# Kernel tuning notes

Measured on AMD Instinct MI355X. Metric: run time of the kernel, lower is better.

Reference implementation:

```python
import jax, jax.numpy as jnp
import numpy as np

N = 50000      # num nodes
EG = 1600000   # num edges (avg degree 32)
IN = 64        # in_dim
OUT = 64       # out_dim
H = 4          # num_heads
D = OUT // H   # per-head dim


def setup_inputs() -> dict:
    key = jax.random.key(0)
    ks = jax.random.split(key, 12)
    s = 1.0 / np.sqrt(IN)
    return {
        "x": jax.random.normal(ks[0], (N, IN), jnp.float32),
        "edge_attr": jax.random.normal(ks[1], (EG, IN), jnp.float32),
        "edge_index": jax.random.randint(ks[2], (2, EG), 0, N, jnp.int32),
        "Wq": jax.random.uniform(ks[3], (OUT, IN), jnp.float32, -s, s),
        "bq": jax.random.uniform(ks[4], (OUT,), jnp.float32, -s, s),
        "Wk": jax.random.uniform(ks[5], (OUT, IN), jnp.float32, -s, s),
        "bk": jax.random.uniform(ks[6], (OUT,), jnp.float32, -s, s),
        "We": jax.random.uniform(ks[7], (OUT, IN), jnp.float32, -s, s),
        "be": jax.random.uniform(ks[8], (OUT,), jnp.float32, -s, s),
        "Wv": jax.random.uniform(ks[9], (OUT, IN), jnp.float32, -s, s),
        "bv": jax.random.uniform(ks[10], (OUT,), jnp.float32, -s, s),
    }


def reference(x, edge_attr, edge_index, Wq, bq, Wk, bk, We, be, Wv, bv):
    n = x.shape[0]
    # linear projections, reshaped to [*, H, D]
    Qh = (x @ Wq.T + bq).reshape(n, H, D)
    Kh = (x @ Wk.T + bk).reshape(n, H, D)
    Vh = (x @ Wv.T + bv).reshape(n, H, D)
    Ee = (edge_attr @ We.T + be).reshape(-1, H, D)
    src = edge_index[0]
    dst = edge_index[1]
    # per-edge score: sum_d K[src] * Q[dst] / sqrt(D) * E  -> [E, H]
    score = ((Kh[src] * Qh[dst]) * (1.0 / np.sqrt(D)) * Ee).sum(-1)
    score = jnp.exp(jnp.clip(score, -5.0, 5.0))            # [E, H]
    msg = Vh[src] * score[..., None]                        # [E, H, D]
    wV = jax.ops.segment_sum(msg, dst, num_segments=n)      # [N, H, D]
    # note: original forward returns wV without dividing by Z
    return wV.reshape(n, H * D)
```

## Files before the change

### kernel.cpp

```cpp
#include <hip/hip_runtime.h>


typedef __attribute__((ext_vector_type(8))) short bf16x8;
typedef __attribute__((ext_vector_type(4))) float f32x4;
union frag_u { uint32_t u[4]; uint4 u4; bf16x8 v; };

__device__ __forceinline__ uint32_t pack2(float a, float b) {
    return (__float_as_uint(a) >> 16) | (__float_as_uint(b) & 0xffff0000u);
}
__device__ __forceinline__ void cvt4(float4 v, uint32_t& h0, uint32_t& h1,
                                     uint32_t& l0, uint32_t& l1) {
    float hx = __uint_as_float(__float_as_uint(v.x) & 0xffff0000u);
    float hy = __uint_as_float(__float_as_uint(v.y) & 0xffff0000u);
    float hz = __uint_as_float(__float_as_uint(v.z) & 0xffff0000u);
    float hw = __uint_as_float(__float_as_uint(v.w) & 0xffff0000u);
    h0 = pack2(v.x, v.y);
    h1 = pack2(v.z, v.w);
    l0 = pack2(v.x - hx, v.y - hy);
    l1 = pack2(v.z - hz, v.w - hw);
}

__global__ __launch_bounds__(256) void proj_kernel(
    const float* __restrict__ x,
    const float* __restrict__ Wq, const float* __restrict__ bq,
    const float* __restrict__ Wk, const float* __restrict__ bk,
    const float* __restrict__ Wv, const float* __restrict__ bv,
    const int* __restrict__ ei, int* __restrict__ cnt,
    float* __restrict__ Qb, float* __restrict__ KV,
    int n, int EG)
{
    __shared__ float WqT[64 * 65];
    __shared__ float WkT[64 * 65];
    __shared__ float WvT[64 * 65];
    __shared__ float xs[4][4][64];

    const int tid  = threadIdx.x;
    const int wave = tid >> 6;
    const int lane = tid & 63;

    #pragma unroll
    for (int k = 0; k < 16; ++k) {
        int idx = tid + k * 256;
        int j = idx >> 6, i = idx & 63;
        WqT[i * 65 + j] = Wq[idx];
        WkT[i * 65 + j] = Wk[idx];
        WvT[i * 65 + j] = Wv[idx];
    }
    const float bqv = bq[lane];
    const float bkv = bk[lane];
    const float bvv = bv[lane];
    __syncthreads();

    for (int blockbase = blockIdx.x * 16; blockbase < n;
         blockbase += gridDim.x * 16) {
        int base = blockbase + wave * 4;
        #pragma unroll
        for (int j = 0; j < 4; ++j) {
            int node = base + j;
            xs[wave][j][lane] = (node < n) ? x[node * 64 + lane] : 0.f;
        }
        __syncthreads();

        float accq[4], acck[4], accv[4];
        #pragma unroll
        for (int j = 0; j < 4; ++j) { accq[j] = bqv; acck[j] = bkv; accv[j] = bvv; }

        #pragma unroll
        for (int f = 0; f < 16; ++f) {
            float wq[4], wk[4], wv[4];
            #pragma unroll
            for (int u = 0; u < 4; ++u) {
                int i = 4 * f + u;
                wq[u] = WqT[i * 65 + lane];
                wk[u] = WkT[i * 65 + lane];
                wv[u] = WvT[i * 65 + lane];
            }
            #pragma unroll
            for (int j = 0; j < 4; ++j) {
                float4 xv = *reinterpret_cast<const float4*>(&xs[wave][j][4 * f]);
                accq[j] = fmaf(xv.x, wq[0], accq[j]);
                accq[j] = fmaf(xv.y, wq[1], accq[j]);
                accq[j] = fmaf(xv.z, wq[2], accq[j]);
                accq[j] = fmaf(xv.w, wq[3], accq[j]);
                acck[j] = fmaf(xv.x, wk[0], acck[j]);
                acck[j] = fmaf(xv.y, wk[1], acck[j]);
                acck[j] = fmaf(xv.z, wk[2], acck[j]);
                acck[j] = fmaf(xv.w, wk[3], acck[j]);
                accv[j] = fmaf(xv.x, wv[0], accv[j]);
                accv[j] = fmaf(xv.y, wv[1], accv[j]);
                accv[j] = fmaf(xv.z, wv[2], accv[j]);
                accv[j] = fmaf(xv.w, wv[3], accv[j]);
            }
        }

        #pragma unroll
        for (int j = 0; j < 4; ++j) {
            int node = base + j;
            if (node < n) {
                Qb[(size_t)node * 64 + lane]       = accq[j];
                KV[(size_t)node * 128 + lane]      = acck[j];
                KV[(size_t)node * 128 + 64 + lane] = accv[j];
            }
        }
        __syncthreads();
    }

    {
        const int nt4 = EG >> 2;
        int i  = blockIdx.x * blockDim.x + threadIdx.x;
        int st = gridDim.x * blockDim.x;
        const int4* d4 = reinterpret_cast<const int4*>(ei + EG);
        for (int e = i; e < nt4; e += st) {
            int4 d = d4[e];
            atomicAdd(&cnt[d.x], 1);
            atomicAdd(&cnt[d.y], 1);
            atomicAdd(&cnt[d.z], 1);
            atomicAdd(&cnt[d.w], 1);
        }
    }
}

__global__ __launch_bounds__(256) void scanA_kernel(
    const int* __restrict__ cnt, int* __restrict__ off,
    int* __restrict__ bsum, int n)
{
    __shared__ int s[256];
    const int t = threadIdx.x;
    const int i = blockIdx.x * 256 + t;
    const int v = (i < n) ? cnt[i] : 0;
    s[t] = v;
    __syncthreads();
    for (int d = 1; d < 256; d <<= 1) {
        int u = (t >= d) ? s[t - d] : 0;
        __syncthreads();
        s[t] += u;
        __syncthreads();
    }
    if (i < n) off[i] = s[t] - v;
    if (t == 255) bsum[blockIdx.x] = s[255];
}

__global__ __launch_bounds__(256) void scanB_kernel(int* __restrict__ bsum, int nb)
{
    __shared__ int s[256];
    const int t = threadIdx.x;
    const int v = (t < nb) ? bsum[t] : 0;
    s[t] = v;
    __syncthreads();
    for (int d = 1; d < 256; d <<= 1) {
        int u = (t >= d) ? s[t - d] : 0;
        __syncthreads();
        s[t] += u;
        __syncthreads();
    }
    if (t < nb) bsum[t] = s[t] - v;
}

__global__ __launch_bounds__(256) void scanC_kernel(
    int* __restrict__ off, const int* __restrict__ bsum,
    int* __restrict__ cursor, int n, int EG)
{
    const int i = blockIdx.x * 256 + threadIdx.x;
    if (i < n) {
        int v = off[i] + bsum[blockIdx.x];
        off[i] = v;
        cursor[i] = v;
    }
    if (i == 0) off[n] = EG;
}

__global__ __launch_bounds__(256) void scatter_kernel(
    const int* __restrict__ ei, int* __restrict__ cursor,
    int* __restrict__ perm, int EG)
{
    int i  = blockIdx.x * blockDim.x + threadIdx.x;
    int st = gridDim.x * blockDim.x;
    for (int e = i; e < EG; e += st) {
        int d = ei[EG + e];
        int p = atomicAdd(&cursor[d], 1);
        perm[p] = e;
    }
}

__global__ __launch_bounds__(256) void agg_kernel(
    const float* __restrict__ ea, const int* __restrict__ ei,
    const int* __restrict__ off, const int* __restrict__ perm,
    const float* __restrict__ Qb, const float* __restrict__ KV,
    const float* __restrict__ We, const float* __restrict__ be,
    float* __restrict__ out, int n, int EG)
{
    __shared__ uint4 bfragLDS[16][64];
    __shared__ int sidt[4][16];
    __shared__ int eidt[4][16];

    const int tid  = threadIdx.x;
    const int wave = __builtin_amdgcn_readfirstlane(tid >> 6);
    const int lane = tid & 63;
    const int g    = lane >> 4;
    const int q    = lane & 15;

    {
        const int nt = wave;
        #pragma unroll
        for (int ks = 0; ks < 2; ++ks) {
            frag_u fh, fl;
            #pragma unroll
            for (int b = 0; b < 2; ++b) {
                float4 w4 = *reinterpret_cast<const float4*>(
                    &We[(size_t)(16 * nt + q) * 64 + 32 * ks + 16 * b + 4 * g]);
                cvt4(w4, fh.u[2 * b + 0], fh.u[2 * b + 1],
                         fl.u[2 * b + 0], fl.u[2 * b + 1]);
            }
            bfragLDS[nt * 4 + ks * 2 + 0][lane] = fh.u4;
            bfragLDS[nt * 4 + ks * 2 + 1][lane] = fl.u4;
        }
    }
    float bias4[4];
    #pragma unroll
    for (int nt = 0; nt < 4; ++nt) bias4[nt] = be[16 * nt + q];
    __syncthreads();

    const int nw  = gridDim.x * 4;
    const int nd4 = n >> 2;

    for (int wid = blockIdx.x * 4 + wave; wid < nd4; wid += nw) {
        const int dbase = wid << 2;
        const int mydst = dbase + g;
        const int j0  = off[mydst];
        const int j1  = off[mydst + 1];
        const int deg = j1 - j0;

        float qreg[4];
        #pragma unroll
        for (int nt = 0; nt < 4; ++nt)
            qreg[nt] = Qb[(size_t)mydst * 64 + 16 * nt + q];

        const int grp  = (lane & 15) >> 2;
        const int slot = lane & 3;
        const int j0p  = __shfl(j0, grp << 4);
        const int j1p  = __shfl(j1, grp << 4);

        int dm = max(deg, __shfl_xor(deg, 16));
        dm = max(dm, __shfl_xor(dm, 32));
        const int iters = __builtin_amdgcn_readfirstlane((dm + 3) >> 2);

        float macc[4] = {0.f, 0.f, 0.f, 0.f};

        for (int c = 0; c < iters; ++c) {
            if (lane < 16) {
                const int  p     = j0p + 4 * c + slot;
                const bool valid = p < j1p;
                const int  eid   = valid ? perm[p] : 0;
                const int  src   = valid ? ei[eid] : -1;
                eidt[wave][lane] = eid;
                sidt[wave][lane] = src;
            }
            __builtin_amdgcn_wave_barrier();

            const int eidq = eidt[wave][q];
            const float* arow = ea + (size_t)eidq * 64;
            frag_u Ah[2], Al[2];
            #pragma unroll
            for (int ks = 0; ks < 2; ++ks) {
                #pragma unroll
                for (int b = 0; b < 2; ++b) {
                    float4 a4 = *reinterpret_cast<const float4*>(
                        &arow[32 * ks + 16 * b + 4 * g]);
                    cvt4(a4, Ah[ks].u[2 * b + 0], Ah[ks].u[2 * b + 1],
                             Al[ks].u[2 * b + 0], Al[ks].u[2 * b + 1]);
                }
            }

            f32x4 acc[4];
            #pragma unroll
            for (int nt = 0; nt < 4; ++nt) {
                acc[nt][0] = bias4[nt]; acc[nt][1] = bias4[nt];
                acc[nt][2] = bias4[nt]; acc[nt][3] = bias4[nt];
                #pragma unroll
                for (int ks = 0; ks < 2; ++ks) {
                    frag_u bh, bl;
                    bh.u4 = bfragLDS[nt * 4 + ks * 2 + 0][lane];
                    bl.u4 = bfragLDS[nt * 4 + ks * 2 + 1][lane];
                    acc[nt] = __builtin_amdgcn_mfma_f32_16x16x32_bf16(
                                  Al[ks].v, bh.v, acc[nt], 0, 0, 0);
                    acc[nt] = __builtin_amdgcn_mfma_f32_16x16x32_bf16(
                                  Ah[ks].v, bl.v, acc[nt], 0, 0, 0);
                    acc[nt] = __builtin_amdgcn_mfma_f32_16x16x32_bf16(
                                  Ah[ks].v, bh.v, acc[nt], 0, 0, 0);
                }
            }

            #pragma unroll
            for (int r = 0; r < 4; ++r) {
                const int srcr = sidt[wave][4 * g + r];
                const float* kb = KV + (size_t)(srcr < 0 ? 0 : srcr) * 128 + q;
                #pragma unroll
                for (int nt = 0; nt < 4; ++nt) {
                    const float kv = kb[16 * nt];
                    const float vv = kb[64 + 16 * nt];
                    float t = kv * qreg[nt] * 0.25f * acc[nt][r];
                    t += __shfl_xor(t, 1);
                    t += __shfl_xor(t, 2);
                    t += __shfl_xor(t, 4);
                    t += __shfl_xor(t, 8);
                    t = fminf(fmaxf(t, -5.f), 5.f);
                    const float s = __expf(t);
                    if (srcr >= 0) macc[nt] = fmaf(vv, s, macc[nt]);
                }
            }
            __builtin_amdgcn_wave_barrier();
        }

        #pragma unroll
        for (int nt = 0; nt < 4; ++nt)
            out[(size_t)mydst * 64 + 16 * nt + q] = macc[nt];
    }
}

extern "C" void kernel_launch(void* const* d_in, const int* in_sizes, int n_in,
                              void* d_out, int out_size, void* d_ws, size_t ws_size,
                              hipStream_t stream) {
    const float* x   = (const float*)d_in[0];
    const float* ea  = (const float*)d_in[1];
    const int*   ei  = (const int*)d_in[2];
    const float* Wq  = (const float*)d_in[3];
    const float* bq  = (const float*)d_in[4];
    const float* Wk  = (const float*)d_in[5];
    const float* bk  = (const float*)d_in[6];
    const float* We  = (const float*)d_in[7];
    const float* be  = (const float*)d_in[8];
    const float* Wv  = (const float*)d_in[9];
    const float* bv  = (const float*)d_in[10];
    float* out = (float*)d_out;

    const int n  = in_sizes[0] / 64;
    const int EG = in_sizes[1] / 64;

    float* Qb   = (float*)d_ws;
    float* KV   = Qb + (size_t)n * 64;
    int* cnt    = (int*)(KV + (size_t)n * 128);
    int* off    = cnt + n;
    int* cursor = off + n + 1;
    int* perm   = cursor + n;
    int* bsum   = perm + EG;

    hipMemsetAsync(cnt, 0, (size_t)n * sizeof(int), stream);

    const int projGrid = (n + 15) / 16;
    proj_kernel<<<projGrid, 256, 0, stream>>>(x, Wq, bq, Wk, bk, Wv, bv,
                                              ei, cnt, Qb, KV, n, EG);

    const int nb = (n + 255) / 256;
    scanA_kernel<<<nb, 256, 0, stream>>>(cnt, off, bsum, n);
    scanB_kernel<<<1, 256, 0, stream>>>(bsum, nb);
    scanC_kernel<<<nb, 256, 0, stream>>>(off, bsum, cursor, n, EG);

    scatter_kernel<<<2048, 256, 0, stream>>>(ei, cursor, perm, EG);

    const int aggGrid = (n / 4 + 3) / 4;
    agg_kernel<<<aggGrid, 256, 0, stream>>>(ea, ei, off, perm,
                                            Qb, KV, We, be, out, n, EG);
}
```

Baseline: 531.5 us.

## Store edge id with source in CSR perm, prefetch edges, merge scans

```diff
diff --git a/kernel.cpp b/kernel.cpp
--- a/kernel.cpp
+++ b/kernel.cpp
@@ -120,78 +120,55 @@
     }
 }
 
-__global__ __launch_bounds__(256) void scanA_kernel(
+__global__ __launch_bounds__(256) void scan_kernel(
     const int* __restrict__ cnt, int* __restrict__ off,
-    int* __restrict__ bsum, int n)
+    int* __restrict__ cursor, int* __restrict__ gtotal, int n)
 {
     __shared__ int s[256];
+    __shared__ int sbase;
     const int t = threadIdx.x;
     const int i = blockIdx.x * 256 + t;
     const int v = (i < n) ? cnt[i] : 0;
     s[t] = v;
     __syncthreads();
+    #pragma unroll
     for (int d = 1; d < 256; d <<= 1) {
         int u = (t >= d) ? s[t - d] : 0;
         __syncthreads();
         s[t] += u;
         __syncthreads();
     }
-    if (i < n) off[i] = s[t] - v;
-    if (t == 255) bsum[blockIdx.x] = s[255];
-}
-
-__global__ __launch_bounds__(256) void scanB_kernel(int* __restrict__ bsum, int nb)
-{
-    __shared__ int s[256];
-    const int t = threadIdx.x;
-    const int v = (t < nb) ? bsum[t] : 0;
-    s[t] = v;
+    if (t == 255) sbase = atomicAdd(gtotal, s[255]);
     __syncthreads();
-    for (int d = 1; d < 256; d <<= 1) {
-        int u = (t >= d) ? s[t - d] : 0;
-        __syncthreads();
-        s[t] += u;
-        __syncthreads();
-    }
-    if (t < nb) bsum[t] = s[t] - v;
-}
-
-__global__ __launch_bounds__(256) void scanC_kernel(
-    int* __restrict__ off, const int* __restrict__ bsum,
-    int* __restrict__ cursor, int n, int EG)
-{
-    const int i = blockIdx.x * 256 + threadIdx.x;
     if (i < n) {
-        int v = off[i] + bsum[blockIdx.x];
-        off[i] = v;
-        cursor[i] = v;
-    }
-    if (i == 0) off[n] = EG;
+        int o = sbase + s[t] - v;
+        off[i]    = o;
+        cursor[i] = o;
+    }
 }
 
 __global__ __launch_bounds__(256) void scatter_kernel(
     const int* __restrict__ ei, int* __restrict__ cursor,
-    int* __restrict__ perm, int EG)
+    int2* __restrict__ perm2, int EG)
 {
     int i  = blockIdx.x * blockDim.x + threadIdx.x;
     int st = gridDim.x * blockDim.x;
     for (int e = i; e < EG; e += st) {
         int d = ei[EG + e];
+        int s = ei[e];
         int p = atomicAdd(&cursor[d], 1);
-        perm[p] = e;
+        perm2[p] = make_int2(e, s);
     }
 }
 
 __global__ __launch_bounds__(256) void agg_kernel(
-    const float* __restrict__ ea, const int* __restrict__ ei,
-    const int* __restrict__ off, const int* __restrict__ perm,
+    const float* __restrict__ ea, const int2* __restrict__ perm2,
+    const int* __restrict__ off, const int* __restrict__ cnt,
     const float* __restrict__ Qb, const float* __restrict__ KV,
     const float* __restrict__ We, const float* __restrict__ be,
-    float* __restrict__ out, int n, int EG)
+    float* __restrict__ out, int n)
 {
     __shared__ uint4 bfragLDS[16][64];
-    __shared__ int sidt[4][16];
-    __shared__ int eidt[4][16];
 
     const int tid  = threadIdx.x;
     const int wave = __builtin_amdgcn_readfirstlane(tid >> 6);
@@ -220,95 +197,103 @@
     for (int nt = 0; nt < 4; ++nt) bias4[nt] = be[16 * nt + q];
     __syncthreads();
 
-    const int nw  = gridDim.x * 4;
-    const int nd4 = n >> 2;
+    const int nw   = gridDim.x * 4;
+    const int nd4  = n >> 2;
+    const int grp  = (lane & 15) >> 2;
+    const int slot = lane & 3;
+    const int coff = lane >> 4;
 
     for (int wid = blockIdx.x * 4 + wave; wid < nd4; wid += nw) {
-        const int dbase = wid << 2;
-        const int mydst = dbase + g;
+        const int mydst = (wid << 2) + g;
         const int j0  = off[mydst];
-        const int j1  = off[mydst + 1];
-        const int deg = j1 - j0;
+        const int cd  = cnt[mydst];
 
         float qreg[4];
         #pragma unroll
         for (int nt = 0; nt < 4; ++nt)
             qreg[nt] = Qb[(size_t)mydst * 64 + 16 * nt + q];
 
-        const int grp  = (lane & 15) >> 2;
-        const int slot = lane & 3;
-        const int j0p  = __shfl(j0, grp << 4);
-        const int j1p  = __shfl(j1, grp << 4);
-
-        int dm = max(deg, __shfl_xor(deg, 16));
+        const int j0p = __shfl(j0, grp << 4);
+        const int j1p = j0p + __shfl(cd, grp << 4);
+
+        int dm = max(cd, __shfl_xor(cd, 16));
         dm = max(dm, __shfl_xor(dm, 32));
         const int iters = __builtin_amdgcn_readfirstlane((dm + 3) >> 2);
+        const int nb    = (iters + 3) >> 2;
 
         float macc[4] = {0.f, 0.f, 0.f, 0.f};
 
-        for (int c = 0; c < iters; ++c) {
-            if (lane < 16) {
-                const int  p     = j0p + 4 * c + slot;
-                const bool valid = p < j1p;
-                const int  eid   = valid ? perm[p] : 0;
-                const int  src   = valid ? ei[eid] : -1;
-                eidt[wave][lane] = eid;
-                sidt[wave][lane] = src;
-            }
-            __builtin_amdgcn_wave_barrier();
-
-            const int eidq = eidt[wave][q];
-            const float* arow = ea + (size_t)eidq * 64;
-            frag_u Ah[2], Al[2];
+        int2 cur = make_int2(0, -1);
+        {
+            const int pl = j0p + 4 * coff + slot;
+            if (pl < j1p) cur = perm2[pl];
+        }
+
+        for (int b = 0; b < nb; ++b) {
+            int2 nxt = make_int2(0, -1);
+            if (b + 1 < nb) {
+                const int pn = j0p + 16 * (b + 1) + 4 * coff + slot;
+                if (pn < j1p) nxt = perm2[pn];
+            }
+            const int maxc2 = iters - 4 * b;
+
             #pragma unroll
-            for (int ks = 0; ks < 2; ++ks) {
-                #pragma unroll
-                for (int b = 0; b < 2; ++b) {
-                    float4 a4 = *reinterpret_cast<const float4*>(
-                        &arow[32 * ks + 16 * b + 4 * g]);
-                    cvt4(a4, Ah[ks].u[2 * b + 0], Ah[ks].u[2 * b + 1],
-                             Al[ks].u[2 * b + 0], Al[ks].u[2 * b + 1]);
+            for (int c2 = 0; c2 < 4; ++c2) {
+                if (c2 < maxc2) {
+                    const int eidq = __shfl(cur.x, (c2 << 4) | q);
+                    const float* arow = ea + (size_t)eidq * 64;
+                    frag_u Ah[2], Al[2];
+                    #pragma unroll
+                    for (int ks = 0; ks < 2; ++ks) {
+                        #pragma unroll
+                        for (int bb = 0; bb < 2; ++bb) {
+                            float4 a4 = *reinterpret_cast<const float4*>(
+                                &arow[32 * ks + 16 * bb + 4 * g]);
+                            cvt4(a4, Ah[ks].u[2 * bb + 0], Ah[ks].u[2 * bb + 1],
+                                     Al[ks].u[2 * bb + 0], Al[ks].u[2 * bb + 1]);
+                        }
+                    }
+
+                    f32x4 acc[4];
+                    #pragma unroll
+                    for (int nt = 0; nt < 4; ++nt) {
+                        acc[nt][0] = bias4[nt]; acc[nt][1] = bias4[nt];
+                        acc[nt][2] = bias4[nt]; acc[nt][3] = bias4[nt];
+                        #pragma unroll
+                        for (int ks = 0; ks < 2; ++ks) {
+                            frag_u bh, bl;
+                            bh.u4 = bfragLDS[nt * 4 + ks * 2 + 0][lane];
+                            bl.u4 = bfragLDS[nt * 4 + ks * 2 + 1][lane];
+                            acc[nt] = __builtin_amdgcn_mfma_f32_16x16x32_bf16(
+                                          Al[ks].v, bh.v, acc[nt], 0, 0, 0);
+                            acc[nt] = __builtin_amdgcn_mfma_f32_16x16x32_bf16(
+                                          Ah[ks].v, bl.v, acc[nt], 0, 0, 0);
+                            acc[nt] = __builtin_amdgcn_mfma_f32_16x16x32_bf16(
+                                          Ah[ks].v, bh.v, acc[nt], 0, 0, 0);
+                        }
+                    }
+
+                    #pragma unroll
+                    for (int r = 0; r < 4; ++r) {
+                        const int srcr = __shfl(cur.y, (c2 << 4) | (g << 2) | r);
+                        const float* kb = KV + (size_t)max(srcr, 0) * 128 + q;
+                        #pragma unroll
+                        for (int nt = 0; nt < 4; ++nt) {
+                            const float kv = kb[16 * nt];
+                            const float vv = kb[64 + 16 * nt];
+                            float t = kv * qreg[nt] * 0.25f * acc[nt][r];
+                            t += __shfl_xor(t, 1);
+                            t += __shfl_xor(t, 2);
+                            t += __shfl_xor(t, 4);
+                            t += __shfl_xor(t, 8);
+                            t = fminf(fmaxf(t, -5.f), 5.f);
+                            const float s = __expf(t);
+                            if (srcr >= 0) macc[nt] = fmaf(vv, s, macc[nt]);
+                        }
+                    }
                 }
             }
-
-            f32x4 acc[4];
-            #pragma unroll
-            for (int nt = 0; nt < 4; ++nt) {
-                acc[nt][0] = bias4[nt]; acc[nt][1] = bias4[nt];
-                acc[nt][2] = bias4[nt]; acc[nt][3] = bias4[nt];
-                #pragma unroll
-                for (int ks = 0; ks < 2; ++ks) {
-                    frag_u bh, bl;
-                    bh.u4 = bfragLDS[nt * 4 + ks * 2 + 0][lane];
-                    bl.u4 = bfragLDS[nt * 4 + ks * 2 + 1][lane];
-                    acc[nt] = __builtin_amdgcn_mfma_f32_16x16x32_bf16(
-                                  Al[ks].v, bh.v, acc[nt], 0, 0, 0);
-                    acc[nt] = __builtin_amdgcn_mfma_f32_16x16x32_bf16(
-                                  Ah[ks].v, bl.v, acc[nt], 0, 0, 0);
-                    acc[nt] = __builtin_amdgcn_mfma_f32_16x16x32_bf16(
-                                  Ah[ks].v, bh.v, acc[nt], 0, 0, 0);
-                }
-            }
-
-            #pragma unroll
-            for (int r = 0; r < 4; ++r) {
-                const int srcr = sidt[wave][4 * g + r];
-                const float* kb = KV + (size_t)(srcr < 0 ? 0 : srcr) * 128 + q;
-                #pragma unroll
-                for (int nt = 0; nt < 4; ++nt) {
-                    const float kv = kb[16 * nt];
-                    const float vv = kb[64 + 16 * nt];
-                    float t = kv * qreg[nt] * 0.25f * acc[nt][r];
-                    t += __shfl_xor(t, 1);
-                    t += __shfl_xor(t, 2);
-                    t += __shfl_xor(t, 4);
-                    t += __shfl_xor(t, 8);
-                    t = fminf(fmaxf(t, -5.f), 5.f);
-                    const float s = __expf(t);
-                    if (srcr >= 0) macc[nt] = fmaf(vv, s, macc[nt]);
-                }
-            }
-            __builtin_amdgcn_wave_barrier();
+            cur = nxt;
         }
 
         #pragma unroll
@@ -336,28 +321,25 @@
     const int n  = in_sizes[0] / 64;
     const int EG = in_sizes[1] / 64;
 
-    float* Qb   = (float*)d_ws;
-    float* KV   = Qb + (size_t)n * 64;
-    int* cnt    = (int*)(KV + (size_t)n * 128);
-    int* off    = cnt + n;
-    int* cursor = off + n + 1;
-    int* perm   = cursor + n;
-    int* bsum   = perm + EG;
-
-    hipMemsetAsync(cnt, 0, (size_t)n * sizeof(int), stream);
-
-    const int projGrid = (n + 15) / 16;
-    proj_kernel<<<projGrid, 256, 0, stream>>>(x, Wq, bq, Wk, bk, Wv, bv,
-                                              ei, cnt, Qb, KV, n, EG);
-
-    const int nb = (n + 255) / 256;
-    scanA_kernel<<<nb, 256, 0, stream>>>(cnt, off, bsum, n);
-    scanB_kernel<<<1, 256, 0, stream>>>(bsum, nb);
-    scanC_kernel<<<nb, 256, 0, stream>>>(off, bsum, cursor, n, EG);
-
-    scatter_kernel<<<2048, 256, 0, stream>>>(ei, cursor, perm, EG);
+    float* Qb    = (float*)d_ws;
+    float* KV    = Qb + (size_t)n * 64;
+    int*   cnt   = (int*)(KV + (size_t)n * 128);
+    int*   gtot  = cnt + n;
+    int*   off   = gtot + 2;
+    int*   cursor= off + n;
+    int2*  perm2 = (int2*)(cursor + n);
+
+    hipMemsetAsync(cnt, 0, (size_t)(n + 1) * sizeof(int), stream);
+
+    proj_kernel<<<512, 256, 0, stream>>>(x, Wq, bq, Wk, bk, Wv, bv,
+                                         ei, cnt, Qb, KV, n, EG);
+
+    const int nbs = (n + 255) / 256;
+    scan_kernel<<<nbs, 256, 0, stream>>>(cnt, off, cursor, gtot, n);
+
+    scatter_kernel<<<2048, 256, 0, stream>>>(ei, cursor, perm2, EG);
 
     const int aggGrid = (n / 4 + 3) / 4;
-    agg_kernel<<<aggGrid, 256, 0, stream>>>(ea, ei, off, perm,
-                                            Qb, KV, We, be, out, n, EG);
-}
+    agg_kernel<<<aggGrid, 256, 0, stream>>>(ea, perm2, off, cnt,
+                                            Qb, KV, We, be, out, n);
+}
```

Result: slower. 681.1 us (+28.2%).
